# Performance work log

Hardware: AMD Instinct MI355X
Metric: run time of the kernel (lower is better)

The kernel has to match this reference:

```python
import jax, jax.numpy as jnp
import numpy as np

D_MODEL = 1024
NUM_HEADS = 16
HEAD_DIM = D_MODEL // NUM_HEADS
B, L = 2, 2048


def setup_inputs() -> dict:
    key = jax.random.key(0)
    ks = jax.random.split(key, 11)
    s = 1.0 / np.sqrt(D_MODEL)
    return {
        "query": jax.random.normal(ks[0], (B, L, D_MODEL), jnp.float32),
        "key": jax.random.normal(ks[1], (B, L, D_MODEL), jnp.float32),
        "value": jax.random.normal(ks[2], (B, L, D_MODEL), jnp.float32),
        "Wq": jax.random.uniform(ks[3], (D_MODEL, D_MODEL), jnp.float32, -s, s),
        "bq": jax.random.uniform(ks[4], (D_MODEL,), jnp.float32, -s, s),
        "Wk": jax.random.uniform(ks[5], (D_MODEL, D_MODEL), jnp.float32, -s, s),
        "bk": jax.random.uniform(ks[6], (D_MODEL,), jnp.float32, -s, s),
        "Wv": jax.random.uniform(ks[7], (D_MODEL, D_MODEL), jnp.float32, -s, s),
        "bv": jax.random.uniform(ks[8], (D_MODEL,), jnp.float32, -s, s),
        "Wo": jax.random.uniform(ks[9], (D_MODEL, D_MODEL), jnp.float32, -s, s),
        "bo": jax.random.uniform(ks[10], (D_MODEL,), jnp.float32, -s, s),
    }


def _split_heads(x):
    b, l, _ = x.shape
    return x.reshape(b, l, NUM_HEADS, HEAD_DIM).transpose(0, 2, 1, 3)  # [B,H,L,Dh]


def reference(query, key, value, Wq, bq, Wk, bk, Wv, bv, Wo, bo):
    Q = _split_heads(query @ Wq.T + bq)
    K = _split_heads(key @ Wk.T + bk)
    V = _split_heads(value @ Wv.T + bv)
    scores = jnp.einsum('bhqd,bhkd->bhqk', Q, K) / jnp.sqrt(jnp.float32(HEAD_DIM))
    attn = jax.nn.softmax(scores, axis=-1)
    ctx = jnp.einsum('bhqk,bhkd->bhqd', attn, V)  # [B,H,L,Dh]
    b, h, l, dh = ctx.shape
    merged = ctx.transpose(0, 2, 1, 3).reshape(b, l, h * dh)
    return merged @ Wo.T + bo
```

## Files before the change

kernel.cpp:

```cpp
#include <hip/hip_runtime.h>

#define B_   2
#define L_   2048
#define D_   1024
#define H_   16
#define DH_  64
#define T_   (B_ * L_)

typedef __bf16 bf16x8 __attribute__((ext_vector_type(8)));
typedef float f32x4 __attribute__((ext_vector_type(4)));
typedef unsigned int u32x4 __attribute__((ext_vector_type(4)));
typedef unsigned short u16x4 __attribute__((ext_vector_type(4)));
typedef unsigned short u16x8 __attribute__((ext_vector_type(8)));

static __device__ __forceinline__ unsigned short f2bf(float x) {
  unsigned int u = __float_as_uint(x);
  u += 0x7fffu + ((u >> 16) & 1u);
  return (unsigned short)(u >> 16);
}

static __device__ __forceinline__ bf16x8 ld_bf8(const unsigned short* p) {
  return __builtin_bit_cast(bf16x8, *reinterpret_cast<const u32x4*>(p));
}

static __device__ __forceinline__ void async_cp16(const unsigned short* g, unsigned short* l) {
  __builtin_amdgcn_global_load_lds(
      (const __attribute__((address_space(1))) unsigned int*)g,
      (__attribute__((address_space(3))) unsigned int*)l,
      16, 0, 0);
}

__global__ void convert_bf16_all(
    const float* __restrict__ q, const float* __restrict__ k, const float* __restrict__ v,
    const float* __restrict__ wq, const float* __restrict__ wk, const float* __restrict__ wv,
    const float* __restrict__ wo, unsigned short* __restrict__ ws) {
  const int M1 = 1 << 20;
  const float* src;
  unsigned short* dst;
  int n;
  switch (blockIdx.y) {
    case 0: src = wq; dst = ws;           n = M1;     break;
    case 1: src = wk; dst = ws + M1;      n = M1;     break;
    case 2: src = wv; dst = ws + 2 * M1;  n = M1;     break;
    case 3: src = wo; dst = ws + 3 * M1;  n = M1;     break;
    case 4: src = q;  dst = ws + 4 * M1;  n = 4 * M1; break;
    case 5: src = k;  dst = ws + 8 * M1;  n = 4 * M1; break;
    default: src = v; dst = ws + 12 * M1; n = 4 * M1; break;
  }
  int i = (blockIdx.x * 256 + threadIdx.x) * 8;
  if (i >= n) return;
  float4 a = *reinterpret_cast<const float4*>(src + i);
  float4 b = *reinterpret_cast<const float4*>(src + i + 4);
  u16x8 o;
  o[0] = f2bf(a.x); o[1] = f2bf(a.y); o[2] = f2bf(a.z); o[3] = f2bf(a.w);
  o[4] = f2bf(b.x); o[5] = f2bf(b.y); o[6] = f2bf(b.z); o[7] = f2bf(b.w);
  *reinterpret_cast<u16x8*>(dst + i) = o;
}

static __device__ __forceinline__ void gemm128_core(
    const unsigned short* __restrict__ A, const unsigned short* __restrict__ Bw,
    int K, int brow, int bcol, unsigned short* As, unsigned short* Bs,
    f32x4 acc[4][4]) {
  const int t = threadIdx.x;
  const int lane = t & 63;
  const int wid = t >> 6;
  const int wr = (wid >> 1) << 6;
  const int wc = (wid & 1) << 6;
  const int lrow = lane & 15;
  const int lko = (lane >> 4) << 3;
  const int r2 = t >> 2;
  const int c8 = (t & 3) << 3;

  f32x4 zero = {0.f, 0.f, 0.f, 0.f};
#pragma unroll
  for (int i = 0; i < 4; ++i)
#pragma unroll
    for (int n = 0; n < 4; ++n) acc[i][n] = zero;

  const unsigned short* ga0 = A + (size_t)(brow + r2) * K + c8;
  const unsigned short* gb0 = Bw + (size_t)(bcol + r2) * K + c8;

  for (int k0 = 0; k0 < K; k0 += 32) {
    __syncthreads();
    async_cp16(ga0 + k0,            &As[r2 * 32 + c8]);
    async_cp16(ga0 + (size_t)64 * K + k0, &As[(64 + r2) * 32 + c8]);
    async_cp16(gb0 + k0,            &Bs[r2 * 32 + c8]);
    async_cp16(gb0 + (size_t)64 * K + k0, &Bs[(64 + r2) * 32 + c8]);
    __syncthreads();

    bf16x8 af[4], bfr[4];
#pragma unroll
    for (int i = 0; i < 4; ++i) af[i] = ld_bf8(&As[(wr + i * 16 + lrow) * 32 + lko]);
#pragma unroll
    for (int n = 0; n < 4; ++n) bfr[n] = ld_bf8(&Bs[(wc + n * 16 + lrow) * 32 + lko]);
#pragma unroll
    for (int i = 0; i < 4; ++i)
#pragma unroll
      for (int n = 0; n < 4; ++n)
        acc[i][n] = __builtin_amdgcn_mfma_f32_16x16x32_bf16(af[i], bfr[n], acc[i][n], 0, 0, 0);
  }
}

__global__ void proj_qkv(
    const unsigned short* __restrict__ xq, const unsigned short* __restrict__ xk,
    const unsigned short* __restrict__ xv, const unsigned short* __restrict__ wqb,
    const unsigned short* __restrict__ wkb, const unsigned short* __restrict__ wvb,
    const float* __restrict__ bq, const float* __restrict__ bk, const float* __restrict__ bv,
    unsigned short* __restrict__ Qb, unsigned short* __restrict__ Kb,
    unsigned short* __restrict__ Vt) {
  __shared__ unsigned short As[128 * 32], Bs[128 * 32];
  const int z = blockIdx.z;
  const unsigned short* A = (z == 0) ? xq : (z == 1) ? xk : xv;
  const unsigned short* W = (z == 0) ? wqb : (z == 1) ? wkb : wvb;
  const float* bias = (z == 0) ? bq : (z == 1) ? bk : bv;
  const int brow = blockIdx.x * 128, bcol = blockIdx.y * 128;

  f32x4 acc[4][4];
  gemm128_core(A, W, D_, brow, bcol, As, Bs, acc);

  const int lane = threadIdx.x & 63;
  const int wid = threadIdx.x >> 6;
  const int wr = (wid >> 1) << 6, wc = (wid & 1) << 6;
  const int lcol = lane & 15, lr4 = (lane >> 4) << 2;

  if (z < 2) {
    unsigned short* Dst = (z == 0) ? Qb : Kb;
    const float scl = (z == 0) ? 0.125f : 1.0f;
#pragma unroll
    for (int i = 0; i < 4; ++i)
#pragma unroll
      for (int n = 0; n < 4; ++n) {
        const int col = bcol + wc + n * 16 + lcol;
        const float bb = bias[col];
        const int h = col >> 6, dh = col & 63;
#pragma unroll
        for (int j = 0; j < 4; ++j) {
          const int row = brow + wr + i * 16 + lr4 + j;
          const int batch = row >> 11, ll = row & 2047;
          Dst[(((size_t)(batch * H_ + h) * L_) + ll) * DH_ + dh] =
              f2bf((acc[i][n][j] + bb) * scl);
        }
      }
  } else {
#pragma unroll
    for (int i = 0; i < 4; ++i)
#pragma unroll
      for (int n = 0; n < 4; ++n) {
        const int col = bcol + wc + n * 16 + lcol;
        const float bb = bias[col];
        const int h = col >> 6, dh = col & 63;
        const int row0 = brow + wr + i * 16 + lr4;
        const int batch = row0 >> 11, ll = row0 & 2047;
        u16x4 pk;
#pragma unroll
        for (int j = 0; j < 4; ++j) pk[j] = f2bf(acc[i][n][j] + bb);
        *reinterpret_cast<u16x4*>(
            &Vt[((size_t)((batch * H_ + h) * DH_ + dh)) * L_ + ll]) = pk;
      }
  }
}

__global__ __launch_bounds__(256, 4) void attn_fwd(
    const unsigned short* __restrict__ Qb,
    const unsigned short* __restrict__ Kb,
    const unsigned short* __restrict__ Vt,
    unsigned short* __restrict__ ctx) {
  __shared__ unsigned short Ks[2][64 * 64];
  __shared__ unsigned short Vs[2][64 * 64];
  __shared__ unsigned short Ps[4][16 * 64];
  const int t = threadIdx.x;
  const int wid = t >> 6, lane = t & 63;
  const int bh = blockIdx.y;
  const int q0 = blockIdx.x * 64 + wid * 16;
  const int lcol = lane & 15;
  const int hi = lane >> 4;
  const int lk = hi << 3;
  const int lr4 = hi << 2;
  const int sxl = (lcol & 7) << 3;

  const unsigned short* Qh = Qb + (size_t)bh * L_ * DH_;
  const unsigned short* Kh = Kb + (size_t)bh * L_ * DH_;
  const unsigned short* Vh = Vt + (size_t)bh * DH_ * L_;

  const int so = t * 8;
  const int sr = t >> 3;
  const int ssw = ((t & 7) * 8) ^ ((sr & 7) << 3);

  bf16x8 qf[2];
#pragma unroll
  for (int kk = 0; kk < 2; ++kk)
    qf[kk] = ld_bf8(Qh + (size_t)(q0 + lcol) * DH_ + kk * 32 + lk);

  bf16x8 ones;
#pragma unroll
  for (int i = 0; i < 8; ++i) ones[i] = (__bf16)1.0f;

  f32x4 zero = {0.f, 0.f, 0.f, 0.f};
  f32x4 o[4];
#pragma unroll
  for (int n = 0; n < 4; ++n) o[n] = zero;
  f32x4 lsum = zero;

  async_cp16(Kh + (size_t)sr * DH_ + ssw,        &Ks[0][so]);
  async_cp16(Kh + (size_t)(sr + 32) * DH_ + ssw, &Ks[0][so + 2048]);
  async_cp16(Vh + (size_t)sr * L_ + ssw,         &Vs[0][so]);
  async_cp16(Vh + (size_t)(sr + 32) * L_ + ssw,  &Vs[0][so + 2048]);
  __syncthreads();

  int cur = 0;
  for (int kv = 0; kv < L_; kv += 64) {
    const int nx = (kv + 64 < L_) ? kv + 64 : 0;
    async_cp16(Kh + (size_t)(nx + sr) * DH_ + ssw,      &Ks[cur ^ 1][so]);
    async_cp16(Kh + (size_t)(nx + sr + 32) * DH_ + ssw, &Ks[cur ^ 1][so + 2048]);
    async_cp16(Vh + (size_t)sr * L_ + nx + ssw,         &Vs[cur ^ 1][so]);
    async_cp16(Vh + (size_t)(sr + 32) * L_ + nx + ssw,  &Vs[cur ^ 1][so + 2048]);

    f32x4 s[4];
#pragma unroll
    for (int n = 0; n < 4; ++n) s[n] = zero;
#pragma unroll
    for (int n = 0; n < 4; ++n)
#pragma unroll
      for (int kk = 0; kk < 2; ++kk) {
        bf16x8 kf = ld_bf8(&Ks[cur][(n * 16 + lcol) * 64 + ((kk * 32 + lk) ^ sxl)]);
        s[n] = __builtin_amdgcn_mfma_f32_16x16x32_bf16(qf[kk], kf, s[n], 0, 0, 0);
      }

#pragma unroll
    for (int n = 0; n < 4; ++n)
#pragma unroll
      for (int j = 0; j < 4; ++j) {
        const int r = lr4 + j;
        Ps[wid][r * 64 + ((n * 16 + lcol) ^ ((r & 7) << 3))] = f2bf(__expf(s[n][j]));
      }

    bf16x8 pf[2];
#pragma unroll
    for (int kk = 0; kk < 2; ++kk)
      pf[kk] = ld_bf8(&Ps[wid][lcol * 64 + ((kk * 32 + lk) ^ sxl)]);

#pragma unroll
    for (int kk = 0; kk < 2; ++kk)
      lsum = __builtin_amdgcn_mfma_f32_16x16x32_bf16(pf[kk], ones, lsum, 0, 0, 0);

#pragma unroll
    for (int kk = 0; kk < 2; ++kk)
#pragma unroll
      for (int n = 0; n < 4; ++n) {
        bf16x8 vf = ld_bf8(&Vs[cur][(n * 16 + lcol) * 64 + ((kk * 32 + lk) ^ sxl)]);
        o[n] = __builtin_amdgcn_mfma_f32_16x16x32_bf16(pf[kk], vf, o[n], 0, 0, 0);
      }

    __syncthreads();
    cur ^= 1;
  }

  const int b = bh >> 4, h = bh & 15;
#pragma unroll
  for (int j = 0; j < 4; ++j) {
    const float inv = 1.0f / lsum[j];
    const int lq = q0 + lr4 + j;
#pragma unroll
    for (int n = 0; n < 4; ++n) {
      const int c = h * DH_ + n * 16 + lcol;
      ctx[((size_t)(b * L_ + lq)) * D_ + c] = f2bf(o[n][j] * inv);
    }
  }
}

__global__ void out_proj(const unsigned short* __restrict__ ctx,
                         const unsigned short* __restrict__ wob,
                         const float* __restrict__ bo, float* __restrict__ out) {
  __shared__ unsigned short As[128 * 32], Bs[128 * 32];
  const int brow = blockIdx.x * 128, bcol = blockIdx.y * 128;
  f32x4 acc[4][4];
  gemm128_core(ctx, wob, D_, brow, bcol, As, Bs, acc);

  const int lane = threadIdx.x & 63;
  const int wid = threadIdx.x >> 6;
  const int wr = (wid >> 1) << 6, wc = (wid & 1) << 6;
  const int lcol = lane & 15, lr4 = (lane >> 4) << 2;
#pragma unroll
  for (int i = 0; i < 4; ++i)
#pragma unroll
    for (int n = 0; n < 4; ++n) {
      const int col = bcol + wc + n * 16 + lcol;
      const float bb = bo[col];
#pragma unroll
      for (int j = 0; j < 4; ++j) {
        const int row = brow + wr + i * 16 + lr4 + j;
        out[(size_t)row * D_ + col] = acc[i][n][j] + bb;
      }
    }
}

extern "C" void kernel_launch(void* const* d_in, const int* in_sizes, int n_in,
                              void* d_out, int out_size, void* d_ws, size_t ws_size,
                              hipStream_t stream) {
  (void)in_sizes; (void)n_in; (void)out_size; (void)ws_size;
  const float* q  = (const float*)d_in[0];
  const float* k  = (const float*)d_in[1];
  const float* v  = (const float*)d_in[2];
  const float* bq = (const float*)d_in[4];
  const float* bk = (const float*)d_in[6];
  const float* bv = (const float*)d_in[8];
  const float* bo = (const float*)d_in[10];
  const float* Wq = (const float*)d_in[3];
  const float* Wk = (const float*)d_in[5];
  const float* Wv = (const float*)d_in[7];
  const float* Wo = (const float*)d_in[9];

  unsigned short* w = (unsigned short*)d_ws;
  const size_t M1 = 1u << 20;
  unsigned short* wqb = w;
  unsigned short* wkb = w + M1;
  unsigned short* wvb = w + 2 * M1;
  unsigned short* wob = w + 3 * M1;
  unsigned short* xq  = w + 4 * M1;
  unsigned short* xk  = w + 8 * M1;
  unsigned short* xv  = w + 12 * M1;
  unsigned short* Qb  = w + 16 * M1;
  unsigned short* Kb  = w + 20 * M1;
  unsigned short* Vt  = w + 24 * M1;
  unsigned short* ctx = w + 28 * M1;
  float* out = (float*)d_out;

  convert_bf16_all<<<dim3(2048, 7), dim3(256), 0, stream>>>(q, k, v, Wq, Wk, Wv, Wo, w);
  proj_qkv<<<dim3(T_ / 128, D_ / 128, 3), dim3(256), 0, stream>>>(
      xq, xk, xv, wqb, wkb, wvb, bq, bk, bv, Qb, Kb, Vt);
  attn_fwd<<<dim3(L_ / 64, B_ * H_), dim3(256), 0, stream>>>(Qb, Kb, Vt, ctx);
  out_proj<<<dim3(T_ / 128, D_ / 128), dim3(256), 0, stream>>>(ctx, wob, bo, out);
}
```

Measured before the change: 231.7 us.

## Double-buffer LDS in projection GEMMs and narrow out_proj tile to 128x64

Replaces the single-buffered GEMM core with a double-buffered version that issues async copies for the next K-slice before computing on the current one. This leaves one barrier per iteration and hides global load latency behind the MFMAs. The output projection switches to 128x64 tiles, doubling its grid from 256 to 512 blocks to fill more CUs. In exchange, the GEMM kernels use twice the LDS, and the narrower tile gives out_proj less reuse per block.

```diff
diff --git a/kernel.cpp b/kernel.cpp
--- a/kernel.cpp
+++ b/kernel.cpp
@@ -57,47 +57,63 @@
   *reinterpret_cast<u16x8*>(dst + i) = o;
 }
 
-static __device__ __forceinline__ void gemm128_core(
+template <int NF>
+static __device__ __forceinline__ void gemm_db(
     const unsigned short* __restrict__ A, const unsigned short* __restrict__ Bw,
     int K, int brow, int bcol, unsigned short* As, unsigned short* Bs,
-    f32x4 acc[4][4]) {
+    f32x4 (&acc)[4][NF]) {
+  constexpr int BSZ = NF * 1024;
   const int t = threadIdx.x;
   const int lane = t & 63;
   const int wid = t >> 6;
   const int wr = (wid >> 1) << 6;
-  const int wc = (wid & 1) << 6;
+  const int wc = (wid & 1) * (NF * 16);
   const int lrow = lane & 15;
   const int lko = (lane >> 4) << 3;
   const int r2 = t >> 2;
   const int c8 = (t & 3) << 3;
+  const int so = t * 8;
 
   f32x4 zero = {0.f, 0.f, 0.f, 0.f};
 #pragma unroll
   for (int i = 0; i < 4; ++i)
 #pragma unroll
-    for (int n = 0; n < 4; ++n) acc[i][n] = zero;
-
-  const unsigned short* ga0 = A + (size_t)(brow + r2) * K + c8;
-  const unsigned short* gb0 = Bw + (size_t)(bcol + r2) * K + c8;
-
+    for (int n = 0; n < NF; ++n) acc[i][n] = zero;
+
+  const unsigned short* ga = A + (size_t)(brow + r2) * K + c8;
+  const unsigned short* gb = Bw + (size_t)(bcol + r2) * K + c8;
+
+  async_cp16(ga,                  &As[so]);
+  async_cp16(ga + (size_t)64 * K, &As[2048 + so]);
+  async_cp16(gb,                  &Bs[so]);
+  if constexpr (NF == 4) async_cp16(gb + (size_t)64 * K, &Bs[2048 + so]);
+  __syncthreads();
+
+  int cur = 0;
   for (int k0 = 0; k0 < K; k0 += 32) {
+    const int nx = (k0 + 32 < K) ? k0 + 32 : 0;
+    unsigned short* Asn = &As[(cur ^ 1) * 4096];
+    unsigned short* Bsn = &Bs[(cur ^ 1) * BSZ];
+    async_cp16(ga + nx,                  &Asn[so]);
+    async_cp16(ga + (size_t)64 * K + nx, &Asn[2048 + so]);
+    async_cp16(gb + nx,                  &Bsn[so]);
+    if constexpr (NF == 4) async_cp16(gb + (size_t)64 * K + nx, &Bsn[2048 + so]);
+
+    const unsigned short* Asc = &As[cur * 4096];
+    const unsigned short* Bsc = &Bs[cur * BSZ];
+    bf16x8 af[4], bfr[NF];
+#pragma unroll
+    for (int i = 0; i < 4; ++i) af[i] = ld_bf8(&Asc[(wr + i * 16 + lrow) * 32 + lko]);
+#pragma unroll
+    for (int n = 0; n < NF; ++n) bfr[n] = ld_bf8(&Bsc[(wc + n * 16 + lrow) * 32 + lko]);
+#pragma unroll
+    for (int i = 0; i < 4; ++i)
+#pragma unroll
+      for (int n = 0; n < NF; ++n)
+        acc[i][n] = __builtin_amdgcn_mfma_f32_16x16x32_bf16(af[i], bfr[n], acc[i][n], 0, 0, 0);
+
     __syncthreads();
-    async_cp16(ga0 + k0,            &As[r2 * 32 + c8]);
-    async_cp16(ga0 + (size_t)64 * K + k0, &As[(64 + r2) * 32 + c8]);
-    async_cp16(gb0 + k0,            &Bs[r2 * 32 + c8]);
-    async_cp16(gb0 + (size_t)64 * K + k0, &Bs[(64 + r2) * 32 + c8]);
-    __syncthreads();
-
-    bf16x8 af[4], bfr[4];
-#pragma unroll
-    for (int i = 0; i < 4; ++i) af[i] = ld_bf8(&As[(wr + i * 16 + lrow) * 32 + lko]);
-#pragma unroll
-    for (int n = 0; n < 4; ++n) bfr[n] = ld_bf8(&Bs[(wc + n * 16 + lrow) * 32 + lko]);
-#pragma unroll
-    for (int i = 0; i < 4; ++i)
-#pragma unroll
-      for (int n = 0; n < 4; ++n)
-        acc[i][n] = __builtin_amdgcn_mfma_f32_16x16x32_bf16(af[i], bfr[n], acc[i][n], 0, 0, 0);
+    cur ^= 1;
   }
 }
 
@@ -108,7 +124,7 @@
     const float* __restrict__ bq, const float* __restrict__ bk, const float* __restrict__ bv,
     unsigned short* __restrict__ Qb, unsigned short* __restrict__ Kb,
     unsigned short* __restrict__ Vt) {
-  __shared__ unsigned short As[128 * 32], Bs[128 * 32];
+  __shared__ unsigned short As[2 * 4096], Bs[2 * 4096];
   const int z = blockIdx.z;
   const unsigned short* A = (z == 0) ? xq : (z == 1) ? xk : xv;
   const unsigned short* W = (z == 0) ? wqb : (z == 1) ? wkb : wvb;
@@ -116,7 +132,7 @@
   const int brow = blockIdx.x * 128, bcol = blockIdx.y * 128;
 
   f32x4 acc[4][4];
-  gemm128_core(A, W, D_, brow, bcol, As, Bs, acc);
+  gemm_db<4>(A, W, D_, brow, bcol, As, Bs, acc);
 
   const int lane = threadIdx.x & 63;
   const int wid = threadIdx.x >> 6;
@@ -145,7 +161,7 @@
 #pragma unroll
     for (int i = 0; i < 4; ++i)
 #pragma unroll
-      for (int n = 0; n < 4; ++n) {
+    for (int n = 0; n < 4; ++n) {
         const int col = bcol + wc + n * 16 + lcol;
         const float bb = bias[col];
         const int h = col >> 6, dh = col & 63;
@@ -271,19 +287,19 @@
 __global__ void out_proj(const unsigned short* __restrict__ ctx,
                          const unsigned short* __restrict__ wob,
                          const float* __restrict__ bo, float* __restrict__ out) {
-  __shared__ unsigned short As[128 * 32], Bs[128 * 32];
-  const int brow = blockIdx.x * 128, bcol = blockIdx.y * 128;
-  f32x4 acc[4][4];
-  gemm128_core(ctx, wob, D_, brow, bcol, As, Bs, acc);
+  __shared__ unsigned short As[2 * 4096], Bs[2 * 2048];
+  const int brow = blockIdx.x * 128, bcol = blockIdx.y * 64;
+  f32x4 acc[4][2];
+  gemm_db<2>(ctx, wob, D_, brow, bcol, As, Bs, acc);
 
   const int lane = threadIdx.x & 63;
   const int wid = threadIdx.x >> 6;
-  const int wr = (wid >> 1) << 6, wc = (wid & 1) << 6;
+  const int wr = (wid >> 1) << 6, wc = (wid & 1) << 5;
   const int lcol = lane & 15, lr4 = (lane >> 4) << 2;
 #pragma unroll
   for (int i = 0; i < 4; ++i)
 #pragma unroll
-    for (int n = 0; n < 4; ++n) {
+    for (int n = 0; n < 2; ++n) {
       const int col = bcol + wc + n * 16 + lcol;
       const float bb = bo[col];
 #pragma unroll
@@ -329,5 +345,5 @@
   proj_qkv<<<dim3(T_ / 128, D_ / 128, 3), dim3(256), 0, stream>>>(
       xq, xk, xv, wqb, wkb, wvb, bq, bk, bv, Qb, Kb, Vt);
   attn_fwd<<<dim3(L_ / 64, B_ * H_), dim3(256), 0, stream>>>(Qb, Kb, Vt, ctx);
-  out_proj<<<dim3(T_ / 128, D_ / 128), dim3(256), 0, stream>>>(ctx, wob, bo, out);
-}
+  out_proj<<<dim3(T_ / 128, D_ / 64), dim3(256), 0, stream>>>(ctx, wob, bo, out);
+}
```

New measurement: 231.2 us. No clear change (-0.2%).
